# Kernel optimization log

Hardware: AMD Instinct MI355X
Metric: run time of the kernel (lower is better)

Reference implementation:

```python
import jax, jax.numpy as jnp
import numpy as np

UNITS = 1024
INPUT_DIM = 2048
OUTPUT_DIM = 1000
EPS = 0.01
DT = 0.1
BATCH = 8192


def _kaiming_like(key, shape, fan_in):
    # matches torch kaiming_uniform_(a=sqrt(5)) bound = sqrt(6/((1+5)*fan_in)) = 1/sqrt(fan_in)
    bound = 1.0 / np.sqrt(fan_in)
    return jax.random.uniform(key, shape, jnp.float32, -bound, bound)


def setup_inputs() -> dict:
    key = jax.random.key(0)
    ks = jax.random.split(key, 12)
    x = jax.random.normal(ks[0], (BATCH, INPUT_DIM), jnp.float32)
    W_in = _kaiming_like(ks[1], (UNITS, INPUT_DIM), INPUT_DIM)
    b_in = _kaiming_like(ks[2], (UNITS,), INPUT_DIM)
    W1 = _kaiming_like(ks[3], (UNITS, UNITS), UNITS)
    b1 = _kaiming_like(ks[4], (UNITS,), UNITS)
    W2 = _kaiming_like(ks[5], (UNITS, UNITS), UNITS)
    b2 = _kaiming_like(ks[6], (UNITS,), UNITS)
    W3 = _kaiming_like(ks[7], (UNITS, UNITS), UNITS)
    b3 = _kaiming_like(ks[8], (UNITS,), UNITS)
    W_out = _kaiming_like(ks[9], (OUTPUT_DIM, UNITS), UNITS)
    b_out = _kaiming_like(ks[10], (OUTPUT_DIM,), UNITS)
    return {"x": x, "W_in": W_in, "b_in": b_in, "W1": W1, "b1": b1,
            "W2": W2, "b2": b2, "W3": W3, "b3": b3,
            "W_out": W_out, "b_out": b_out}


def transnet_layer(z, W, b):
    # z: (B, 2U). Implicit layer: A y = rhs, output = C y - rhs (== -y mathematically)
    U = W.shape[0]
    u_in, v_in = z[:, :U], z[:, U:]
    relu_u = jax.nn.relu(u_in)
    rhs_u = u_in + DT * b                      # (B, U)
    rhs_v = v_in + (DT / EPS) * relu_u         # (B, U)
    rhs = jnp.concatenate([rhs_u, rhs_v], axis=1)  # (B, 2U)
    eye = jnp.eye(U, dtype=z.dtype)
    A = jnp.block([[eye, DT * W],
                   [-DT * W.T, (1.0 + DT / EPS) * eye]])  # (2U, 2U), batch-independent
    # factor once, solve against all batch rhs columns at once
    y = jnp.linalg.solve(A, rhs.T).T           # (B, 2U)
    u, v = y[:, :U], y[:, U:]
    u_out = DT * (v @ W.T) - u_in - DT * b
    v_out = -DT * (u @ W) + (DT / EPS) * v - v_in - (DT / EPS) * relu_u
    return jnp.concatenate([u_out, v_out], axis=1)


def reference(x, W_in, b_in, W1, b1, W2, b2, W3, b3, W_out, b_out):
    z = x @ W_in.T + b_in                      # (B, U)
    z = jnp.concatenate([z, jax.nn.relu(z)], axis=1)  # (B, 2U)
    z = transnet_layer(z, W1, b1)
    z = transnet_layer(z, W2, b2)
    z = transnet_layer(z, W3, b3)
    z = z[:, :UNITS]
    logits = jax.nn.softmax(z @ W_out.T + b_out, axis=1)
    return logits
```

## Files before the change

kernel.cpp:

```cpp
#include <hip/hip_runtime.h>
#include <hip/hip_bf16.h>
#include <cstdint>


typedef __bf16 bf16;
typedef __bf16 bf16x4 __attribute__((ext_vector_type(4)));
typedef __bf16 bf16x8 __attribute__((ext_vector_type(8)));
typedef float  f32x4  __attribute__((ext_vector_type(4)));

#define C_DT    0.1f
#define C_DTEPS 10.0f
#define C_DINV  (1.0f/11.0f)
#define C_MSC   (0.01f/121.0f)

__device__ __forceinline__ void async_load16(const bf16* g, bf16* l) {
    __builtin_amdgcn_global_load_lds(
        (__attribute__((address_space(1))) void*)(g),
        (__attribute__((address_space(3))) void*)(l),
        16, 0, 0);
}

__device__ __forceinline__ void remap_block(int& bx, int& by) {
    if (gridDim.y == 64) {
        const int lin  = by * 8 + bx;
        const int xcd  = lin & 7;
        const int slot = lin >> 3;
        by = xcd * 8 + (slot & 7);
        bx = slot >> 3;
    }
}

template<int EPI>
__global__ __launch_bounds__(256, 3)
void gemm_bt(const bf16* __restrict__ A, const bf16* __restrict__ B,
             float* __restrict__ out_f,
             bf16* __restrict__ out_b1, bf16* __restrict__ out_b2,
             const float* __restrict__ e0, const float* __restrict__ e1,
             const float* __restrict__ e2,
             int M, int N, int K, int lda, int ldb,
             int ldf, int ld1, int ld2, float sgn,
             long zsA, long zsB, long zs1, long zs2)
{
    __shared__ __attribute__((aligned(16))) char smem[32768];
    bf16* sAe = (bf16*)smem;
    bf16* sBe = (bf16*)(smem + 16384);

    const int t    = threadIdx.x;
    const int wave = t >> 6;
    const int lane = t & 63;
    int bx = blockIdx.x, by = blockIdx.y;
    remap_block(bx, by);
    const long zb = blockIdx.z;
    A += zb * zsA;
    B += zb * zsB;
    if (out_b1) out_b1 += zb * zs1;
    if (out_b2) out_b2 += zb * zs2;

    const long row0 = (long)by * 128;
    const long col0 = (long)bx * 128;
    const int wr = wave >> 1, wc = wave & 1;

    f32x4 acc[4][4];
#pragma unroll
    for (int i = 0; i < 4; i++)
#pragma unroll
        for (int j = 0; j < 4; j++)
            acc[i][j] = f32x4{0.f, 0.f, 0.f, 0.f};

    const int  q  = t >> 2;
    const int  gp = ((t & 3) + 4 - ((q + (q >> 2)) & 3)) & 3;
    const bf16* gA = A + (row0 + q) * (long)lda + gp * 8;
    const bf16* gB = B + (col0 + q) * (long)ldb + gp * 8;

    const int l15  = lane & 15;
    const int fch  = ((lane >> 4) + l15 + (l15 >> 2)) & 3;
    const int aoff = (wr * 64 + l15) * 32 + fch * 8;
    const int boff = (wc * 64 + l15) * 32 + fch * 8;

    auto stage = [&](int buf, int k0) {
        bf16* dA = sAe + buf * 4096 + wave * 512;
        bf16* dB = sBe + buf * 4096 + wave * 512;
        async_load16(gA + k0,                     dA);
        async_load16(gA + 64 * (long)lda + k0,    dA + 2048);
        async_load16(gB + k0,                     dB);
        async_load16(gB + 64 * (long)ldb + k0,    dB + 2048);
    };

    const int nIter = K >> 5;
    stage(0, 0);
    __syncthreads();
    for (int k = 0; k < nIter; k++) {
        const int cur = k & 1;
        if (k + 1 < nIter) stage(cur ^ 1, (k + 1) << 5);

        bf16x8 af[4], bfv[4];
#pragma unroll
        for (int i = 0; i < 4; i++)
            af[i] = *(const bf16x8*)(sAe + cur * 4096 + aoff + i * 16 * 32);
#pragma unroll
        for (int j = 0; j < 4; j++)
            bfv[j] = *(const bf16x8*)(sBe + cur * 4096 + boff + j * 16 * 32);
#pragma unroll
        for (int i = 0; i < 4; i++)
#pragma unroll
            for (int j = 0; j < 4; j++)
                acc[i][j] = __builtin_amdgcn_mfma_f32_16x16x32_bf16(
                    af[i], bfv[j], acc[i][j], 0, 0, 0);

        __syncthreads();
    }

    float* epi = (float*)smem + wave * 1024;
    const int wbase = (lane >> 4) * 256 + (l15 >> 2) * 4 + (l15 & 3);

#pragma unroll
    for (int i = 0; i < 4; i++) {
#pragma unroll
        for (int j = 0; j < 4; j++)
#pragma unroll
            for (int r = 0; r < 4; r++)
                epi[wbase + r * 64 + 16 * j] = acc[i][j][r];

#pragma unroll
        for (int qq = 0; qq < 4; qq++) {
            const f32x4 a4 = ((const f32x4*)epi)[qq * 64 + lane];
            const long m = row0 + wr * 64 + i * 16 + qq * 4 + (lane >> 4);
            const long n = col0 + wc * 64 + 4 * l15;

            if (EPI == 2) {
                bf16x4 ov, o2;
#pragma unroll
                for (int e = 0; e < 4; e++) {
                    ov[e] = (bf16)(sgn * a4[e]);
                    o2[e] = (bf16)(C_DT * sgn * a4[e]);
                }
                *(bf16x4*)(out_b1 + m * (long)ld1 + n) = ov;
                if (out_b2) *(bf16x4*)(out_b2 + m * (long)ld2 + n) = o2;
            } else {
                const f32x4 u0 = *(const f32x4*)(e0 + m * (long)ldf + n);
                const f32x4 b1 = *(const f32x4*)(e1 + n);
                bf16x4 hv, lv;
#pragma unroll
                for (int e = 0; e < 4; e++) {
                    float un = sgn * a4[e] - u0[e] - C_DT * b1[e];
                    bf16 h = (bf16)un;
                    hv[e] = h;
                    lv[e] = (bf16)(un - (float)h);
                }
                *(bf16x4*)(out_b1 + m * (long)ld1 + n) = hv;
                *(bf16x4*)(out_b2 + m * (long)ld2 + n) = lv;
            }
        }
    }
}

__global__ __launch_bounds__(256, 3)
void gemm_z0m(const bf16* __restrict__ xb, const bf16* __restrict__ winb,
              const bf16* __restrict__ wtbf,
              float* __restrict__ u, bf16* __restrict__ ACa,
              bf16* __restrict__ Minv,
              const float* __restrict__ e1, const float* __restrict__ e2)
{
    __shared__ __attribute__((aligned(16))) char smem[32768];
    bf16* sAe = (bf16*)smem;
    bf16* sBe = (bf16*)(smem + 16384);

    const int t    = threadIdx.x;
    const int wave = t >> 6;
    const int lane = t & 63;
    const long M1v = 1024L * 1024;

    const bool mainp = (blockIdx.y < 64);
    int bx, by, nIter, zm = 0;
    long lda;
    const bf16 *Abase, *Bbase;
    if (mainp) {
        const int lin  = blockIdx.y * 8 + blockIdx.x;
        const int xcd  = lin & 7;
        const int slot = lin >> 3;
        by = xcd * 8 + (slot & 7);
        bx = slot >> 3;
        lda = 2048; nIter = 64;
        Abase = xb; Bbase = winb;
    } else {
        zm = (blockIdx.y - 64) >> 3;
        by = (blockIdx.y - 64) & 7;
        bx = blockIdx.x;
        lda = 1024; nIter = 32;
        Abase = wtbf + zm * M1v; Bbase = Abase;
    }
    const long row0 = (long)by * 128;
    const long col0 = (long)bx * 128;
    const int wr = wave >> 1, wc = wave & 1;

    f32x4 acc[4][4];
#pragma unroll
    for (int i = 0; i < 4; i++)
#pragma unroll
        for (int j = 0; j < 4; j++)
            acc[i][j] = f32x4{0.f, 0.f, 0.f, 0.f};

    const int  q  = t >> 2;
    const int  gp = ((t & 3) + 4 - ((q + (q >> 2)) & 3)) & 3;
    const bf16* gA = Abase + (row0 + q) * lda + gp * 8;
    const bf16* gB = Bbase + (col0 + q) * lda + gp * 8;

    const int l15  = lane & 15;
    const int fch  = ((lane >> 4) + l15 + (l15 >> 2)) & 3;
    const int aoff = (wr * 64 + l15) * 32 + fch * 8;
    const int boff = (wc * 64 + l15) * 32 + fch * 8;

    auto stage = [&](int buf, int k0) {
        bf16* dA = sAe + buf * 4096 + wave * 512;
        bf16* dB = sBe + buf * 4096 + wave * 512;
        async_load16(gA + k0,              dA);
        async_load16(gA + 64 * lda + k0,   dA + 2048);
        async_load16(gB + k0,              dB);
        async_load16(gB + 64 * lda + k0,   dB + 2048);
    };

    stage(0, 0);
    __syncthreads();
    for (int k = 0; k < nIter; k++) {
        const int cur = k & 1;
        if (k + 1 < nIter) stage(cur ^ 1, (k + 1) << 5);

        bf16x8 af[4], bfv[4];
#pragma unroll
        for (int i = 0; i < 4; i++)
            af[i] = *(const bf16x8*)(sAe + cur * 4096 + aoff + i * 16 * 32);
#pragma unroll
        for (int j = 0; j < 4; j++)
            bfv[j] = *(const bf16x8*)(sBe + cur * 4096 + boff + j * 16 * 32);
#pragma unroll
        for (int i = 0; i < 4; i++)
#pragma unroll
            for (int j = 0; j < 4; j++)
                acc[i][j] = __builtin_amdgcn_mfma_f32_16x16x32_bf16(
                    af[i], bfv[j], acc[i][j], 0, 0, 0);
        __syncthreads();
    }

    float* epi = (float*)smem + wave * 1024;
    const int wbase = (lane >> 4) * 256 + (l15 >> 2) * 4 + (l15 & 3);

#pragma unroll
    for (int i = 0; i < 4; i++) {
#pragma unroll
        for (int j = 0; j < 4; j++)
#pragma unroll
            for (int r = 0; r < 4; r++)
                epi[wbase + r * 64 + 16 * j] = acc[i][j][r];

#pragma unroll
        for (int qq = 0; qq < 4; qq++) {
            const f32x4 a4 = ((const f32x4*)epi)[qq * 64 + lane];
            const long m = row0 + wr * 64 + i * 16 + qq * 4 + (lane >> 4);
            const long n = col0 + wc * 64 + 4 * l15;

            if (mainp) {
                const f32x4 b1 = *(const f32x4*)(e1 + n);
                const f32x4 b2 = *(const f32x4*)(e2 + n);
                f32x4 tv; bf16x4 rv, hv;
#pragma unroll
                for (int e = 0; e < 4; e++) {
                    tv[e] = a4[e] + b1[e];
                    rv[e] = (bf16)(11.f * fmaxf(tv[e], 0.f));
                    hv[e] = (bf16)(tv[e] + C_DT * b2[e]);
                }
                *(f32x4*)(u + m * 1024 + n)           = tv;
                *(bf16x4*)(ACa + m * 2048 + n)        = rv;
                *(bf16x4*)(ACa + m * 2048 + 1024 + n) = hv;
            } else {
                bf16x4 ov;
#pragma unroll
                for (int e = 0; e < 4; e++)
                    ov[e] = (bf16)(((m == n + e) ? C_DINV : 0.f) - C_MSC * a4[e]);
                *(bf16x4*)(Minv + zm * M1v + m * 1024 + n) = ov;
            }
        }
    }
}

__global__ __launch_bounds__(256, 3)
void pp2a(const bf16* __restrict__ Minv, const bf16* __restrict__ Wbf,
          bf16* __restrict__ Bcat, bf16* __restrict__ Pmat,
          bf16* __restrict__ Ccat)
{
    __shared__ __attribute__((aligned(16))) char smem[32768];
    bf16* sAe = (bf16*)smem;
    bf16* sBe = (bf16*)(smem + 16384);

    const int bid  = blockIdx.x;
    const int t    = threadIdx.x;
    const int wave = t >> 6;
    const int lane = t & 63;
    const long M1v = 1024L * 1024;

    const bf16 *A, *B;
    bf16 *o1, *o2 = nullptr;
    bf16 *bhi = nullptr;
    int ld1 = 2048;
    float s1;

    const int z6  = bid >> 6;
    const int idx = bid & 63;
    const int bx = idx & 7, by = idx >> 3;
    if (z6 < 3) {
        A = Minv + z6 * M1v; B = Wbf + z6 * M1v;
        o1 = Bcat + z6 * 2 * M1v + 1024; s1 = C_DT;
        bhi = Bcat + z6 * 2 * M1v;
    } else {
        const int zr = z6 - 3;
        A = Wbf + zr * M1v; B = Minv + zr * M1v;
        o1 = Pmat + zr * M1v; ld1 = 1024; s1 = 1.f;
        o2 = Ccat + zr * 2 * M1v;
    }

    const long row0 = (long)by * 128;
    const long col0 = (long)bx * 128;
    const int wr = wave >> 1, wc = wave & 1;

    if (bhi) {
        const int rr = t >> 1, cc = (t & 1) * 64;
#pragma unroll
        for (int s = 0; s < 8; s++) {
            const long src = (row0 + rr) * 1024 + col0 + cc + s * 8;
            *(bf16x8*)(bhi + (row0 + rr) * 2048 + col0 + cc + s * 8) =
                *(const bf16x8*)(A + src);
        }
    }

    f32x4 acc[4][4];
#pragma unroll
    for (int i = 0; i < 4; i++)
#pragma unroll
        for (int j = 0; j < 4; j++)
            acc[i][j] = f32x4{0.f, 0.f, 0.f, 0.f};

    const int  q  = t >> 2;
    const int  gp = ((t & 3) + 4 - ((q + (q >> 2)) & 3)) & 3;
    const bf16* gA = A + (row0 + q) * 1024 + gp * 8;
    const bf16* gB = B + (col0 + q) * 1024 + gp * 8;

    const int l15  = lane & 15;
    const int fch  = ((lane >> 4) + l15 + (l15 >> 2)) & 3;
    const int aoff = (wr * 64 + l15) * 32 + fch * 8;
    const int boff = (wc * 64 + l15) * 32 + fch * 8;

    auto stage = [&](int buf, int k0) {
        bf16* dA = sAe + buf * 4096 + wave * 512;
        bf16* dB = sBe + buf * 4096 + wave * 512;
        async_load16(gA + k0,              dA);
        async_load16(gA + 64 * 1024 + k0,  dA + 2048);
        async_load16(gB + k0,              dB);
        async_load16(gB + 64 * 1024 + k0,  dB + 2048);
    };

    stage(0, 0);
    __syncthreads();
    for (int k = 0; k < 32; k++) {
        const int cur = k & 1;
        if (k + 1 < 32) stage(cur ^ 1, (k + 1) << 5);

        bf16x8 af[4], bfv[4];
#pragma unroll
        for (int i = 0; i < 4; i++)
            af[i] = *(const bf16x8*)(sAe + cur * 4096 + aoff + i * 16 * 32);
#pragma unroll
        for (int j = 0; j < 4; j++)
            bfv[j] = *(const bf16x8*)(sBe + cur * 4096 + boff + j * 16 * 32);
#pragma unroll
        for (int i = 0; i < 4; i++)
#pragma unroll
            for (int j = 0; j < 4; j++)
                acc[i][j] = __builtin_amdgcn_mfma_f32_16x16x32_bf16(
                    af[i], bfv[j], acc[i][j], 0, 0, 0);
        __syncthreads();
    }

    float* epi = (float*)smem + wave * 1024;
    const int wbase = (lane >> 4) * 256 + (l15 >> 2) * 4 + (l15 & 3);

#pragma unroll
    for (int i = 0; i < 4; i++) {
#pragma unroll
        for (int j = 0; j < 4; j++)
#pragma unroll
            for (int r = 0; r < 4; r++)
                epi[wbase + r * 64 + 16 * j] = acc[i][j][r];

#pragma unroll
        for (int qq = 0; qq < 4; qq++) {
            const f32x4 a4 = ((const f32x4*)epi)[qq * 64 + lane];
            const long m = row0 + wr * 64 + i * 16 + qq * 4 + (lane >> 4);
            const long n = col0 + wc * 64 + 4 * l15;
            bf16x4 ov;
#pragma unroll
            for (int e = 0; e < 4; e++) ov[e] = (bf16)(s1 * a4[e]);
            *(bf16x4*)(o1 + m * (long)ld1 + n) = ov;
            if (o2) {
                bf16x4 o2v;
#pragma unroll
                for (int e = 0; e < 4; e++) o2v[e] = (bf16)(C_DT * a4[e]);
                *(bf16x4*)(o2 + m * 2048 + n) = o2v;
            }
        }
    }
}

__global__ __launch_bounds__(256, 2)
void gemm_layer(const bf16* __restrict__ A, const bf16* __restrict__ B1,
                const bf16* __restrict__ B2, float* __restrict__ u,
                bf16* __restrict__ ACo,
                const float* __restrict__ bl, const float* __restrict__ bn)
{
    __shared__ __attribute__((aligned(16))) char smem[49152];
    bf16* sA  = (bf16*)smem;
    bf16* sB1 = (bf16*)(smem + 16384);
    bf16* sB2 = (bf16*)(smem + 32768);

    const int t    = threadIdx.x;
    const int wave = t >> 6;
    const int lane = t & 63;
    int bx = blockIdx.x, by = blockIdx.y;
    remap_block(bx, by);
    const long row0 = (long)by * 128;
    const long col0 = (long)bx * 128;
    const int wr = wave >> 1, wc = wave & 1;

    f32x4 accU[4][4], accV[4][4];
#pragma unroll
    for (int i = 0; i < 4; i++)
#pragma unroll
        for (int j = 0; j < 4; j++) {
            accU[i][j] = f32x4{0.f, 0.f, 0.f, 0.f};
            accV[i][j] = f32x4{0.f, 0.f, 0.f, 0.f};
        }

    const int  q  = t >> 2;
    const int  gp = ((t & 3) + 4 - ((q + (q >> 2)) & 3)) & 3;
    const bf16* gA  = A  + (row0 + q) * 2048 + gp * 8;
    const bf16* gB1 = B1 + (col0 + q) * 2048 + gp * 8;
    const bf16* gB2 = B2 + (col0 + q) * 2048 + gp * 8;

    const int l15  = lane & 15;
    const int fch  = ((lane >> 4) + l15 + (l15 >> 2)) & 3;
    const int aoff = (wr * 64 + l15) * 32 + fch * 8;
    const int boff = (wc * 64 + l15) * 32 + fch * 8;

    auto stage = [&](int buf, int k0) {
        bf16* dA  = sA  + buf * 4096 + wave * 512;
        bf16* dB1 = sB1 + buf * 4096 + wave * 512;
        bf16* dB2 = sB2 + buf * 4096 + wave * 512;
        async_load16(gA  + k0,             dA);
        async_load16(gA  + 64 * 2048 + k0, dA + 2048);
        async_load16(gB1 + k0,             dB1);
        async_load16(gB1 + 64 * 2048 + k0, dB1 + 2048);
        async_load16(gB2 + k0,             dB2);
        async_load16(gB2 + 64 * 2048 + k0, dB2 + 2048);
    };

    stage(0, 0);
    __syncthreads();
    for (int k = 0; k < 64; k++) {
        const int cur = k & 1;
        if (k + 1 < 64) stage(cur ^ 1, (k + 1) << 5);

        bf16x8 af[4], b1v[4], b2v[4];
#pragma unroll
        for (int i = 0; i < 4; i++)
            af[i] = *(const bf16x8*)(sA + cur * 4096 + aoff + i * 16 * 32);
#pragma unroll
        for (int j = 0; j < 4; j++) {
            b1v[j] = *(const bf16x8*)(sB1 + cur * 4096 + boff + j * 16 * 32);
            b2v[j] = *(const bf16x8*)(sB2 + cur * 4096 + boff + j * 16 * 32);
        }
#pragma unroll
        for (int i = 0; i < 4; i++)
#pragma unroll
            for (int j = 0; j < 4; j++) {
                accV[i][j] = __builtin_amdgcn_mfma_f32_16x16x32_bf16(
                    af[i], b1v[j], accV[i][j], 0, 0, 0);
                accU[i][j] = __builtin_amdgcn_mfma_f32_16x16x32_bf16(
                    af[i], b2v[j], accU[i][j], 0, 0, 0);
            }
        __syncthreads();
    }

    float* epi = (float*)smem + wave * 1024;
    const int wbase = (lane >> 4) * 256 + (l15 >> 2) * 4 + (l15 & 3);

#pragma unroll
    for (int i = 0; i < 4; i++) {
#pragma unroll
        for (int j = 0; j < 4; j++)
#pragma unroll
            for (int r = 0; r < 4; r++)
                epi[wbase + r * 64 + 16 * j] = accV[i][j][r];
        f32x4 v4[4];
#pragma unroll
        for (int qq = 0; qq < 4; qq++)
            v4[qq] = ((const f32x4*)epi)[qq * 64 + lane];
#pragma unroll
        for (int j = 0; j < 4; j++)
#pragma unroll
            for (int r = 0; r < 4; r++)
                epi[wbase + r * 64 + 16 * j] = accU[i][j][r];

#pragma unroll
        for (int qq = 0; qq < 4; qq++) {
            const f32x4 a4 = ((const f32x4*)epi)[qq * 64 + lane];
            const long m  = row0 + wr * 64 + i * 16 + qq * 4 + (lane >> 4);
            const long n  = col0 + wc * 64 + 4 * l15;
            const long iu = m * 1024 + n;
            const f32x4 u0 = *(const f32x4*)(u + iu);
            const f32x4 c1 = *(const f32x4*)(bl + n);
            const f32x4 c2 = *(const f32x4*)(bn + n);
            f32x4 un; bf16x4 rv, hv;
#pragma unroll
            for (int e = 0; e < 4; e++) {
                un[e] = a4[e] - u0[e] - C_DT * c1[e];
                rv[e] = (bf16)(C_DTEPS * fmaxf(un[e], 0.f) - v4[qq][e]);
                hv[e] = (bf16)(un[e] + C_DT * c2[e]);
            }
            *(f32x4*)(u + iu) = un;
            *(bf16x4*)(ACo + m * 2048 + n)        = rv;
            *(bf16x4*)(ACo + m * 2048 + 1024 + n) = hv;
        }
    }
}

__global__ __launch_bounds__(256, 2)
void gemm_split(const bf16* __restrict__ Ah, const bf16* __restrict__ Al,
                const bf16* __restrict__ Bh, const bf16* __restrict__ Bl,
                float* __restrict__ out, const float* __restrict__ bias,
                int M, int N, int K, int blim)
{
    __shared__ __attribute__((aligned(16))) char smem[65536];
    bf16* sAh = (bf16*)smem;
    bf16* sAl = (bf16*)(smem + 16384);
    bf16* sBh = (bf16*)(smem + 32768);
    bf16* sBl = (bf16*)(smem + 49152);

    const int t    = threadIdx.x;
    const int wave = t >> 6;
    const int lane = t & 63;
    int bx = blockIdx.x, by = blockIdx.y;
    remap_block(bx, by);
    const long row0 = (long)by * 128;
    const long col0 = (long)bx * 128;
    const int wr = wave >> 1, wc = wave & 1;

    f32x4 acc[4][4];
#pragma unroll
    for (int i = 0; i < 4; i++)
#pragma unroll
        for (int j = 0; j < 4; j++)
            acc[i][j] = f32x4{0.f, 0.f, 0.f, 0.f};

    const int  q  = t >> 2;
    const int  gp = ((t & 3) + 4 - ((q + (q >> 2)) & 3)) & 3;
    const long gao = (row0 + q) * (long)K + gp * 8;
    const long gbo = (col0 + q) * (long)K + gp * 8;

    const int l15  = lane & 15;
    const int fch  = ((lane >> 4) + l15 + (l15 >> 2)) & 3;
    const int aoff = (wr * 64 + l15) * 32 + fch * 8;
    const int boff = (wc * 64 + l15) * 32 + fch * 8;

    auto stage = [&](int buf, int k0) {
        const int d = buf * 4096 + wave * 512;
        async_load16(Ah + gao + k0,                 sAh + d);
        async_load16(Ah + gao + 64 * (long)K + k0,  sAh + d + 2048);
        async_load16(Al + gao + k0,                 sAl + d);
        async_load16(Al + gao + 64 * (long)K + k0,  sAl + d + 2048);
        async_load16(Bh + gbo + k0,                 sBh + d);
        async_load16(Bh + gbo + 64 * (long)K + k0,  sBh + d + 2048);
        async_load16(Bl + gbo + k0,                 sBl + d);
        async_load16(Bl + gbo + 64 * (long)K + k0,  sBl + d + 2048);
    };

    const int nIter = K >> 5;
    stage(0, 0);
    __syncthreads();
    for (int k = 0; k < nIter; k++) {
        const int cur = k & 1;
        if (k + 1 < nIter) stage(cur ^ 1, (k + 1) << 5);

        bf16x8 ah[4], al[4], bh[4], bl[4];
#pragma unroll
        for (int i = 0; i < 4; i++) {
            ah[i] = *(const bf16x8*)(sAh + cur * 4096 + aoff + i * 16 * 32);
            al[i] = *(const bf16x8*)(sAl + cur * 4096 + aoff + i * 16 * 32);
        }
#pragma unroll
        for (int j = 0; j < 4; j++) {
            bh[j] = *(const bf16x8*)(sBh + cur * 4096 + boff + j * 16 * 32);
            bl[j] = *(const bf16x8*)(sBl + cur * 4096 + boff + j * 16 * 32);
        }
#pragma unroll
        for (int i = 0; i < 4; i++)
#pragma unroll
            for (int j = 0; j < 4; j++) {
                acc[i][j] = __builtin_amdgcn_mfma_f32_16x16x32_bf16(
                    ah[i], bh[j], acc[i][j], 0, 0, 0);
                acc[i][j] = __builtin_amdgcn_mfma_f32_16x16x32_bf16(
                    ah[i], bl[j], acc[i][j], 0, 0, 0);
                acc[i][j] = __builtin_amdgcn_mfma_f32_16x16x32_bf16(
                    al[i], bh[j], acc[i][j], 0, 0, 0);
            }
        __syncthreads();
    }

    float* epi = (float*)smem + wave * 1024;
    const int wbase = (lane >> 4) * 256 + (l15 >> 2) * 4 + (l15 & 3);

#pragma unroll
    for (int i = 0; i < 4; i++) {
#pragma unroll
        for (int j = 0; j < 4; j++)
#pragma unroll
            for (int r = 0; r < 4; r++)
                epi[wbase + r * 64 + 16 * j] = acc[i][j][r];

#pragma unroll
        for (int qq = 0; qq < 4; qq++) {
            f32x4 a4 = ((const f32x4*)epi)[qq * 64 + lane];
            const long m = row0 + wr * 64 + i * 16 + qq * 4 + (lane >> 4);
            const long n = col0 + wc * 64 + 4 * l15;
            f32x4 bv = f32x4{0.f, 0.f, 0.f, 0.f};
            if (n < blim) bv = *(const f32x4*)(bias + n);
#pragma unroll
            for (int e = 0; e < 4; e++) a4[e] += bv[e];
            *(f32x4*)(out + m * (long)N + n) = a4;
        }
    }
}

__global__ __launch_bounds__(256)
void prep_all(const float* __restrict__ x, bf16* __restrict__ xb,
              const float* __restrict__ win, bf16* __restrict__ winb,
              const float* __restrict__ wout, bf16* __restrict__ wouth,
              bf16* __restrict__ woutl,
              const float* __restrict__ w0, const float* __restrict__ w1,
              const float* __restrict__ w2,
              bf16* __restrict__ Wb, bf16* __restrict__ Wtb)
{
    __shared__ float tile[32][33];
    const long bid = blockIdx.x;
    const int  t   = threadIdx.x;

    if (bid < 16384) {
        const long i4 = bid * 256 + t;
        const f32x4 v = ((const f32x4*)x)[i4];
        bf16x4 o;
#pragma unroll
        for (int e = 0; e < 4; e++) o[e] = (bf16)v[e];
        ((bf16x4*)xb)[i4] = o;
    } else if (bid < 18432) {
        const long i4 = (bid - 16384) * 256 + t;
        const f32x4 v = ((const f32x4*)win)[i4];
        bf16x4 o;
#pragma unroll
        for (int e = 0; e < 4; e++) o[e] = (bf16)v[e];
        ((bf16x4*)winb)[i4] = o;
    } else if (bid < 19456) {
        const long i4   = (bid - 18432) * 256 + t;
        const long base = i4 * 4;
        const int  nrow = (int)(base >> 10);
        bf16x4 h, l;
        if (nrow < 1000) {
            const f32x4 v = ((const f32x4*)wout)[i4];
#pragma unroll
            for (int e = 0; e < 4; e++) {
                bf16 hh = (bf16)v[e];
                h[e] = hh;
                l[e] = (bf16)(v[e] - (float)hh);
            }
        } else {
#pragma unroll
            for (int e = 0; e < 4; e++) { h[e] = (bf16)0.f; l[e] = (bf16)0.f; }
        }
        ((bf16x4*)wouth)[i4] = h;
        ((bf16x4*)woutl)[i4] = l;
    } else {
        const long b2 = bid - 19456;
        const int  z  = (int)(b2 >> 10);
        const int  idx = (int)(b2 & 1023);
        const float* W = (z == 0) ? w0 : (z == 1) ? w1 : w2;
        const long zo = (long)z << 20;
        const int bxt = (idx & 31) * 32, byt = (idx >> 5) * 32;
        const int tx = t & 31, ty = t >> 5;
#pragma unroll
        for (int i = 0; i < 32; i += 8) {
            float v = W[(long)(byt + ty + i) * 1024 + bxt + tx];
            tile[ty + i][tx] = v;
            Wb[zo + (long)(byt + ty + i) * 1024 + bxt + tx] = (bf16)v;
        }
        __syncthreads();
#pragma unroll
        for (int i = 0; i < 32; i += 8)
            Wtb[zo + (long)(bxt + ty + i) * 1024 + byt + tx] = (bf16)tile[tx][ty + i];
    }
}

__global__ __launch_bounds__(256)
void softmax_rows(const float* __restrict__ logits, float* __restrict__ out)
{
    const int row = blockIdx.x;
    const float* lp = logits + (long)row * 1024;
    const int t = threadIdx.x;
    float v[4];
    float mx = -1e30f;
#pragma unroll
    for (int i = 0; i < 4; i++) {
        const int c = t + i * 256;
        v[i] = (c < 1000) ? lp[c] : -1e30f;
        mx = fmaxf(mx, v[i]);
    }
#pragma unroll
    for (int off = 32; off; off >>= 1)
        mx = fmaxf(mx, __shfl_xor(mx, off));
    __shared__ float sm[4], ss[4];
    const int wave = t >> 6;
    if ((t & 63) == 0) sm[wave] = mx;
    __syncthreads();
    mx = fmaxf(fmaxf(sm[0], sm[1]), fmaxf(sm[2], sm[3]));
    float sum = 0.f;
#pragma unroll
    for (int i = 0; i < 4; i++) {
        v[i] = __expf(v[i] - mx);
        sum += v[i];
    }
#pragma unroll
    for (int off = 32; off; off >>= 1)
        sum += __shfl_xor(sum, off);
    if ((t & 63) == 0) ss[wave] = sum;
    __syncthreads();
    const float inv = 1.f / (ss[0] + ss[1] + ss[2] + ss[3]);
#pragma unroll
    for (int i = 0; i < 4; i++) {
        const int c = t + i * 256;
        if (c < 1000) out[(long)row * 1000 + c] = v[i] * inv;
    }
}

extern "C" void kernel_launch(void* const* d_in, const int* in_sizes, int n_in,
                              void* d_out, int out_size, void* d_ws, size_t ws_size,
                              hipStream_t stream)
{
    const float* x     = (const float*)d_in[0];
    const float* W_in  = (const float*)d_in[1];
    const float* b_in  = (const float*)d_in[2];
    const float* Ws[3] = {(const float*)d_in[3], (const float*)d_in[5], (const float*)d_in[7]};
    const float* bs[3] = {(const float*)d_in[4], (const float*)d_in[6], (const float*)d_in[8]};
    const float* W_out = (const float*)d_in[9];
    const float* b_out = (const float*)d_in[10];
    float* out = (float*)d_out;

    char* ws = (char*)d_ws;
    const size_t MB = 1u << 20;
    const long M1 = 1024L * 1024;
    bf16*  xb    = (bf16*)(ws);
    bf16*  zh    = (bf16*)(ws);
    bf16*  zl    = (bf16*)(ws + 16 * MB);
    bf16*  Bcat  = (bf16*)(ws + 18 * MB);
    bf16*  Winb  = (bf16*)(ws + 32 * MB);
    bf16*  Wouth = (bf16*)(ws + 36 * MB);
    bf16*  Woutl = (bf16*)(ws + 38 * MB);
    bf16*  Wbf   = (bf16*)(ws + 40 * MB);
    bf16*  Ccat  = (bf16*)(ws + 46 * MB);
    float* u     = (float*)(ws + 58 * MB);
    float* logits= (float*)(ws + 58 * MB);
    bf16*  AC_a  = (bf16*)(ws + 90 * MB);
    bf16*  AC_b  = (bf16*)(ws + 122 * MB);
    bf16*  Wtbf  = (bf16*)(ws + 122 * MB);
    bf16*  Minv  = (bf16*)(ws + 128 * MB);
    bf16*  Pmat  = (bf16*)(ws + 134 * MB);

    const dim3 blk(256);
    const dim3 gBig(8, 64);
    const dim3 gZ0(8, 88);
    const dim3 gSm3(8, 8, 3);

    prep_all<<<22528, blk, 0, stream>>>(x, xb, W_in, Winb, W_out, Wouth, Woutl,
                                        Ws[0], Ws[1], Ws[2], Wbf, Wtbf);

    gemm_z0m<<<gZ0, blk, 0, stream>>>(xb, Winb, Wtbf, u, AC_a, Minv,
                                      b_in, bs[0]);

    pp2a<<<384, blk, 0, stream>>>(Minv, Wbf, Bcat, Pmat, Ccat);

    gemm_bt<2><<<gSm3, blk, 0, stream>>>(Pmat, Wbf, nullptr, Ccat + 1024, nullptr,
                                         nullptr, nullptr, nullptr,
                                         1024, 1024, 1024, 1024, 1024,
                                         0, 2048, 0, 0.01f, M1, M1, 2 * M1, 0);

    gemm_layer<<<gBig, blk, 0, stream>>>(AC_a, Bcat, Ccat, u, AC_b, bs[0], bs[1]);
    gemm_layer<<<gBig, blk, 0, stream>>>(AC_b, Bcat + 2 * M1, Ccat + 2 * M1,
                                         u, AC_a, bs[1], bs[2]);
    gemm_bt<5><<<gBig, blk, 0, stream>>>(AC_a, Ccat + 4 * M1, nullptr, zh, zl,
                                         u, bs[2], nullptr,
                                         8192, 1024, 2048, 2048, 2048,
                                         1024, 1024, 1024, 1.f, 0, 0, 0, 0);

    gemm_split<<<gBig, blk, 0, stream>>>(zh, zl, Wouth, Woutl, logits, b_out,
                                         8192, 1024, 1024, 1000);
    softmax_rows<<<8192, blk, 0, stream>>>(logits, out);
}
```

Baseline: 492.8 us.

## Replace dependent P*W GEMM with Gram-matrix path to remove a kernel launch

Previously the fourth block of the per-layer matrix (W*Minv*W style product) was computed by a separate GEMM after pp2a produced Pmat. Now gemm_z0m also computes the Gram matrix W*W^T in extra blocks, and pp2b derives that block algebraically from G and G*G products in the same launch as the other precompute GEMMs. This removes one serial kernel launch and dependency stage, in exchange for extra GEMM blocks in the first kernel and a different bf16 rounding path.

Result: faster. 478.8 us (-2.9%).

```diff
diff --git a/kernel.cpp b/kernel.cpp
--- a/kernel.cpp
+++ b/kernel.cpp
@@ -12,6 +12,8 @@
 #define C_DTEPS 10.0f
 #define C_DINV  (1.0f/11.0f)
 #define C_MSC   (0.01f/121.0f)
+#define SC_G1   (0.01f/11.0f)
+#define SC_G2   (0.0001f/121.0f)
 
 __device__ __forceinline__ void async_load16(const bf16* g, bf16* l) {
     __builtin_amdgcn_global_load_lds(
@@ -127,16 +129,7 @@
             const long m = row0 + wr * 64 + i * 16 + qq * 4 + (lane >> 4);
             const long n = col0 + wc * 64 + 4 * l15;
 
-            if (EPI == 2) {
-                bf16x4 ov, o2;
-#pragma unroll
-                for (int e = 0; e < 4; e++) {
-                    ov[e] = (bf16)(sgn * a4[e]);
-                    o2[e] = (bf16)(C_DT * sgn * a4[e]);
-                }
-                *(bf16x4*)(out_b1 + m * (long)ld1 + n) = ov;
-                if (out_b2) *(bf16x4*)(out_b2 + m * (long)ld2 + n) = o2;
-            } else {
+            if (EPI == 5) {
                 const f32x4 u0 = *(const f32x4*)(e0 + m * (long)ldf + n);
                 const f32x4 b1 = *(const f32x4*)(e1 + n);
                 bf16x4 hv, lv;
@@ -156,9 +149,9 @@
 
 __global__ __launch_bounds__(256, 3)
 void gemm_z0m(const bf16* __restrict__ xb, const bf16* __restrict__ winb,
-              const bf16* __restrict__ wtbf,
+              const bf16* __restrict__ wtbf, const bf16* __restrict__ wbf,
               float* __restrict__ u, bf16* __restrict__ ACa,
-              bf16* __restrict__ Minv,
+              bf16* __restrict__ Minv, bf16* __restrict__ Gmat,
               const float* __restrict__ e1, const float* __restrict__ e2)
 {
     __shared__ __attribute__((aligned(16))) char smem[32768];
@@ -171,6 +164,7 @@
     const long M1v = 1024L * 1024;
 
     const bool mainp = (blockIdx.y < 64);
+    bool isG = false;
     int bx, by, nIter, zm = 0;
     long lda;
     const bf16 *Abase, *Bbase;
@@ -183,11 +177,13 @@
         lda = 2048; nIter = 64;
         Abase = xb; Bbase = winb;
     } else {
-        zm = (blockIdx.y - 64) >> 3;
-        by = (blockIdx.y - 64) & 7;
+        const int ty = blockIdx.y - 64;
+        isG = (ty >= 24);
+        zm = (isG ? ty - 24 : ty) >> 3;
+        by = ty & 7;
         bx = blockIdx.x;
         lda = 1024; nIter = 32;
-        Abase = wtbf + zm * M1v; Bbase = Abase;
+        Abase = (isG ? wbf : wtbf) + zm * M1v; Bbase = Abase;
     }
     const long row0 = (long)by * 128;
     const long col0 = (long)bx * 128;
@@ -271,6 +267,11 @@
                 *(f32x4*)(u + m * 1024 + n)           = tv;
                 *(bf16x4*)(ACa + m * 2048 + n)        = rv;
                 *(bf16x4*)(ACa + m * 2048 + 1024 + n) = hv;
+            } else if (isG) {
+                bf16x4 ov;
+#pragma unroll
+                for (int e = 0; e < 4; e++) ov[e] = (bf16)a4[e];
+                *(bf16x4*)(Gmat + zm * M1v + m * 1024 + n) = ov;
             } else {
                 bf16x4 ov;
 #pragma unroll
@@ -283,9 +284,9 @@
 }
 
 __global__ __launch_bounds__(256, 3)
-void pp2a(const bf16* __restrict__ Minv, const bf16* __restrict__ Wbf,
-          bf16* __restrict__ Bcat, bf16* __restrict__ Pmat,
-          bf16* __restrict__ Ccat)
+void pp2b(const bf16* __restrict__ Minv, const bf16* __restrict__ Wbf,
+          const bf16* __restrict__ Gmat,
+          bf16* __restrict__ Bcat, bf16* __restrict__ Ccat)
 {
     __shared__ __attribute__((aligned(16))) char smem[32768];
     bf16* sAe = (bf16*)smem;
@@ -297,24 +298,27 @@
     const int lane = t & 63;
     const long M1v = 1024L * 1024;
 
+    int role, z, idx;
+    if (bid < 128)      { role = 0; z = bid >> 6;          idx = bid & 63; }
+    else if (bid < 320) { role = 1; z = (bid - 128) >> 6;  idx = (bid - 128) & 63; }
+    else                { role = 2; z = (bid - 320) >> 6;  idx = (bid - 320) & 63; }
+    const int bx = idx & 7, by = idx >> 3;
+
     const bf16 *A, *B;
-    bf16 *o1, *o2 = nullptr;
+    bf16 *o1;
     bf16 *bhi = nullptr;
-    int ld1 = 2048;
-    float s1;
-
-    const int z6  = bid >> 6;
-    const int idx = bid & 63;
-    const int bx = idx & 7, by = idx >> 3;
-    if (z6 < 3) {
-        A = Minv + z6 * M1v; B = Wbf + z6 * M1v;
-        o1 = Bcat + z6 * 2 * M1v + 1024; s1 = C_DT;
-        bhi = Bcat + z6 * 2 * M1v;
+    const bf16* Gsrc = nullptr;
+    if (role == 0) {
+        A = Minv + z * M1v; B = Wbf + z * M1v;
+        o1 = Bcat + z * 2 * M1v + 1024;
+        bhi = Bcat + z * 2 * M1v;
+    } else if (role == 1) {
+        A = Wbf + z * M1v; B = Minv + z * M1v;
+        o1 = Ccat + z * 2 * M1v;
     } else {
-        const int zr = z6 - 3;
-        A = Wbf + zr * M1v; B = Minv + zr * M1v;
-        o1 = Pmat + zr * M1v; ld1 = 1024; s1 = 1.f;
-        o2 = Ccat + zr * 2 * M1v;
+        A = Gmat + z * M1v; B = A;
+        o1 = Ccat + z * 2 * M1v + 1024;
+        Gsrc = A;
     }
 
     const long row0 = (long)by * 128;
@@ -396,15 +400,16 @@
             const long m = row0 + wr * 64 + i * 16 + qq * 4 + (lane >> 4);
             const long n = col0 + wc * 64 + 4 * l15;
             bf16x4 ov;
-#pragma unroll
-            for (int e = 0; e < 4; e++) ov[e] = (bf16)(s1 * a4[e]);
-            *(bf16x4*)(o1 + m * (long)ld1 + n) = ov;
-            if (o2) {
-                bf16x4 o2v;
-#pragma unroll
-                for (int e = 0; e < 4; e++) o2v[e] = (bf16)(C_DT * a4[e]);
-                *(bf16x4*)(o2 + m * 2048 + n) = o2v;
+            if (role == 2) {
+                const bf16x4 g4 = *(const bf16x4*)(Gsrc + m * 1024 + n);
+#pragma unroll
+                for (int e = 0; e < 4; e++)
+                    ov[e] = (bf16)(SC_G1 * (float)g4[e] - SC_G2 * a4[e]);
+            } else {
+#pragma unroll
+                for (int e = 0; e < 4; e++) ov[e] = (bf16)(C_DT * a4[e]);
             }
+            *(bf16x4*)(o1 + m * 2048 + n) = ov;
         }
     }
 }
@@ -777,25 +782,19 @@
     bf16*  AC_b  = (bf16*)(ws + 122 * MB);
     bf16*  Wtbf  = (bf16*)(ws + 122 * MB);
     bf16*  Minv  = (bf16*)(ws + 128 * MB);
-    bf16*  Pmat  = (bf16*)(ws + 134 * MB);
+    bf16*  Gmat  = (bf16*)(ws + 134 * MB);
 
     const dim3 blk(256);
     const dim3 gBig(8, 64);
-    const dim3 gZ0(8, 88);
-    const dim3 gSm3(8, 8, 3);
+    const dim3 gZ0(8, 112);
 
     prep_all<<<22528, blk, 0, stream>>>(x, xb, W_in, Winb, W_out, Wouth, Woutl,
                                         Ws[0], Ws[1], Ws[2], Wbf, Wtbf);
 
-    gemm_z0m<<<gZ0, blk, 0, stream>>>(xb, Winb, Wtbf, u, AC_a, Minv,
-                                      b_in, bs[0]);
-
-    pp2a<<<384, blk, 0, stream>>>(Minv, Wbf, Bcat, Pmat, Ccat);
-
-    gemm_bt<2><<<gSm3, blk, 0, stream>>>(Pmat, Wbf, nullptr, Ccat + 1024, nullptr,
-                                         nullptr, nullptr, nullptr,
-                                         1024, 1024, 1024, 1024, 1024,
-                                         0, 2048, 0, 0.01f, M1, M1, 2 * M1, 0);
+    gemm_z0m<<<gZ0, blk, 0, stream>>>(xb, Winb, Wtbf, Wbf, u, AC_a,
+                                      Minv, Gmat, b_in, bs[0]);
+
+    pp2b<<<512, blk, 0, stream>>>(Minv, Wbf, Gmat, Bcat, Ccat);
 
     gemm_layer<<<gBig, blk, 0, stream>>>(AC_a, Bcat, Ccat, u, AC_b, bs[0], bs[1]);
     gemm_layer<<<gBig, blk, 0, stream>>>(AC_b, Bcat + 2 * M1, Ccat + 2 * M1,
```
